# Optimization experiments

Measured on AMD Instinct MI355X. Metric: run time of the kernel, lower is better.

Reference implementation:

```python
import jax, jax.numpy as jnp
import numpy as np

N, E, IN, HID, H, OUT = 50000, 800000, 128, 64, 4, 128
NEG = 0.2   # LeakyReLU slope in GATv2
EPS = 1e-5  # BatchNorm eps


def _seg_softmax(a, seg, n):
    # numerically stable softmax over edges grouped by destination node
    amax = jax.lax.stop_gradient(jax.ops.segment_max(a, seg, num_segments=n))
    amax = jnp.where(jnp.isfinite(amax), amax, 0.0)
    ex = jnp.exp(a - amax[seg])
    den = jax.ops.segment_sum(ex, seg, num_segments=n)
    return ex / (den[seg] + 1e-16)


def _gatv2(x, src, dst, e_attr, Wl, bl, Wr, br, We, att, bias, heads, c, concat):
    n = x.shape[0]
    xl = (x @ Wl + bl).reshape(n, heads, c)   # source transform (x_j)
    xr = (x @ Wr + br).reshape(n, heads, c)   # target transform (x_i)
    ee = (e_attr @ We).reshape(-1, heads, c)  # edge feature transform
    m = xl[src] + xr[dst] + ee                # [E, H, C]
    m = jnp.where(m > 0, m, NEG * m)          # LeakyReLU
    alpha = _seg_softmax(jnp.einsum('ehc,hc->eh', m, att), dst, n)  # [E, H]
    out = jax.ops.segment_sum(alpha[:, :, None] * xl[src], dst, num_segments=n)
    out = out.reshape(n, heads * c) if concat else out.mean(axis=1)
    return out + bias


def _bn(h, g, b):  # BatchNorm1d, training-mode batch stats (biased var)
    mu = jnp.mean(h, axis=0)
    var = jnp.var(h, axis=0)
    return (h - mu) * jax.lax.rsqrt(var + EPS) * g + b


def _prelu(h, a):
    return jnp.where(h > 0, h, a * h)


def setup_inputs() -> dict:
    key = jax.random.key(0)
    ks = jax.random.split(key, 16)
    def nrm(k, shape, fan):
        return jax.random.normal(k, shape, jnp.float32) / np.float32(np.sqrt(fan))
    x = jax.random.normal(ks[0], (N, IN), jnp.float32)
    edge_index = jax.random.randint(ks[1], (2, E), 0, N, jnp.int32)
    edge_attr = jax.random.uniform(ks[2], (E, 1), dtype=jnp.float32)
    return {
        'x': x, 'edge_index': edge_index, 'edge_attr': edge_attr,
        # layer 1: heads=4, concat=True
        'Wl1': nrm(ks[3], (IN, H * HID), IN), 'bl1': jnp.zeros((H * HID,), jnp.float32),
        'Wr1': nrm(ks[4], (IN, H * HID), IN), 'br1': jnp.zeros((H * HID,), jnp.float32),
        'We1': nrm(ks[5], (1, H * HID), 1),
        'att1': nrm(ks[6], (H, HID), HID),
        'cb1': jnp.zeros((H * HID,), jnp.float32),
        'bng1': jnp.ones((H * HID,), jnp.float32), 'bnb1': jnp.zeros((H * HID,), jnp.float32),
        'pa': jnp.float32(0.25),  # PReLU single parameter (shared by both uses)
        # layer 2: heads=1, concat=False
        'Wl2': nrm(ks[7], (H * HID, OUT), H * HID), 'bl2': jnp.zeros((OUT,), jnp.float32),
        'Wr2': nrm(ks[8], (H * HID, OUT), H * HID), 'br2': jnp.zeros((OUT,), jnp.float32),
        'We2': nrm(ks[9], (1, OUT), 1),
        'att2': nrm(ks[10], (1, OUT), OUT),
        'cb2': jnp.zeros((OUT,), jnp.float32),
        'bng2': jnp.ones((OUT,), jnp.float32), 'bnb2': jnp.zeros((OUT,), jnp.float32),
        'skipW': nrm(ks[11], (IN, OUT), IN), 'skipb': jnp.zeros((OUT,), jnp.float32),
    }


def reference(x, edge_index, edge_attr, Wl1, bl1, Wr1, br1, We1, att1, cb1,
              bng1, bnb1, pa, Wl2, bl2, Wr2, br2, We2, att2, cb2, bng2, bnb2,
              skipW, skipb):
    src, dst = edge_index[0], edge_index[1]
    h = _gatv2(x, src, dst, edge_attr, Wl1, bl1, Wr1, br1, We1, att1, cb1, H, HID, True)
    h = _prelu(_bn(h, bng1, bnb1), pa)  # dropout = identity (eval)
    h = _gatv2(h, src, dst, edge_attr, Wl2, bl2, Wr2, br2, We2, att2, cb2, 1, OUT, False)
    h = _prelu(_bn(h, bng2, bnb2), pa)
    return h + (x @ skipW + skipb)
```

## Files before the change

kernel.cpp:

```cpp
#include <hip/hip_runtime.h>
#include <cstdint>
#include <cstddef>

#define NNODES 50000
#define NEDGES 800000
#define DH1    256
#define DOUT   128

typedef unsigned short u16;
typedef __bf16 bf16x8 __attribute__((ext_vector_type(8)));
typedef float  f32x4  __attribute__((ext_vector_type(4)));

__device__ __forceinline__ float bf2f(unsigned int u) {
  union { unsigned int i; float f; } x; x.i = u << 16; return x.f;
}
__device__ __forceinline__ u16 f2bf(float f) {
  union { float f; unsigned int i; } x; x.f = f;
  unsigned int r = x.i + 0x7fffu + ((x.i >> 16) & 1u);
  return (u16)(r >> 16);
}
__device__ __forceinline__ void dec8(uint4 r, float* o) {
  o[0] = bf2f(r.x & 0xffffu); o[1] = bf2f(r.x >> 16);
  o[2] = bf2f(r.y & 0xffffu); o[3] = bf2f(r.y >> 16);
  o[4] = bf2f(r.z & 0xffffu); o[5] = bf2f(r.z >> 16);
  o[6] = bf2f(r.w & 0xffffu); o[7] = bf2f(r.w >> 16);
}
__device__ __forceinline__ uint4 pack8(const float* v) {
  uint4 p;
  p.x = (unsigned)f2bf(v[0]) | ((unsigned)f2bf(v[1]) << 16);
  p.y = (unsigned)f2bf(v[2]) | ((unsigned)f2bf(v[3]) << 16);
  p.z = (unsigned)f2bf(v[4]) | ((unsigned)f2bf(v[5]) << 16);
  p.w = (unsigned)f2bf(v[6]) | ((unsigned)f2bf(v[7]) << 16);
  return p;
}


#define CNT_BLKS 3125
#define CVT_BLKS 6250
#define W1_BLKS  320
#define W2_BLKS  256

__global__ __launch_bounds__(256) void setup_k(
    const int* __restrict__ dst, int* __restrict__ cnt,
    const float* __restrict__ x, u16* __restrict__ xbf,
    const float* __restrict__ Wl1, const float* __restrict__ Wr1,
    const float* __restrict__ bl1, const float* __restrict__ br1,
    const float* __restrict__ Wl2, const float* __restrict__ Wr2,
    const float* __restrict__ bl2, const float* __restrict__ br2,
    const float* __restrict__ skW, const float* __restrict__ skb,
    const float* __restrict__ att1, const float* __restrict__ We1,
    const float* __restrict__ att2, const float* __restrict__ We2,
    u16* __restrict__ Wcat1, float* __restrict__ bias1,
    u16* __restrict__ Wt2, float* __restrict__ bias2,
    float* __restrict__ axw) {
  int b = blockIdx.x, t = threadIdx.x;
  if (b < CNT_BLKS) {
    int e = b * 256 + t;
    if (e < NEDGES) atomicAdd(&cnt[dst[e]], 1);
  } else if (b < CNT_BLKS + CVT_BLKS) {
    int i = ((b - CNT_BLKS) * 256 + t) * 4;
    float4 v = *reinterpret_cast<const float4*>(x + i);
    uint2 pk;
    pk.x = (unsigned)f2bf(v.x) | ((unsigned)f2bf(v.y) << 16);
    pk.y = (unsigned)f2bf(v.z) | ((unsigned)f2bf(v.w) << 16);
    *reinterpret_cast<uint2*>(xbf + i) = pk;
  } else if (b < CNT_BLKS + CVT_BLKS + W1_BLKS) {
    int idx = (b - CNT_BLKS - CVT_BLKS) * 256 + t;
    if (idx < 640) bias1[idx] = idx < 256 ? bl1[idx] : idx < 512 ? br1[idx - 256] : skb[idx - 512];
    int n = idx >> 7, k = idx & 127;
    float v = n < 256 ? Wl1[k * 256 + n] : n < 512 ? Wr1[k * 256 + (n - 256)] : skW[k * 128 + (n - 512)];
    Wcat1[idx] = f2bf(v);
  } else if (b < CNT_BLKS + CVT_BLKS + W1_BLKS + W2_BLKS) {
    int idx = (b - CNT_BLKS - CVT_BLKS - W1_BLKS) * 256 + t;
    if (idx < 256) bias2[idx] = idx < 128 ? bl2[idx] : br2[idx - 128];
    int n = idx >> 8, k = idx & 255;
    float v = n < 128 ? Wl2[k * 128 + n] : Wr2[k * 128 + (n - 128)];
    Wt2[idx] = f2bf(v);
  } else {
    if (t < 4) {
      float s = 0.f;
      for (int c = 0; c < 64; ++c) s += att1[t * 64 + c] * We1[t * 64 + c];
      axw[t] = s;
    } else if (t == 4) {
      float s = 0.f;
      for (int c = 0; c < 128; ++c) s += att2[c] * We2[c];
      axw[4] = s;
    }
  }
}


__global__ __launch_bounds__(256) void offsets_k(const int* __restrict__ cnt, int* __restrict__ offs,
                                                 int* __restrict__ cursor, int* __restrict__ total) {
  int i = blockIdx.x * 256 + threadIdx.x;
  int lane = threadIdx.x & 63;
  int c = (i < NNODES) ? cnt[i] : 0;
  int incl = c;
  #pragma unroll
  for (int d = 1; d < 64; d <<= 1) {
    int t = __shfl_up(incl, d, 64);
    if (lane >= d) incl += t;
  }
  int wtotal = __shfl(incl, 63, 64);
  int base = 0;
  if (lane == 63) base = atomicAdd(total, wtotal);
  base = __shfl(base, 63, 64);
  int off = base + incl - c;
  if (i < NNODES) { offs[i] = off; cursor[i] = off; }
}

__global__ __launch_bounds__(256) void scatter_k(const int* __restrict__ src, const int* __restrict__ dst,
                                                 const float* __restrict__ ea, int* __restrict__ cursor,
                                                 int2* __restrict__ epair) {
  int e = blockIdx.x * 256 + threadIdx.x;
  if (e >= NEDGES) return;
  int d = dst[e];
  int p = atomicAdd(&cursor[d], 1);
  int2 v; v.x = src[e]; v.y = __float_as_int(ea[e]);
  epair[p] = v;
}


template<int K, int B1, int B2, int LDC0, int LDC1, int LDC2, int SPAN, int ATTLEN, bool DO_ATT>
__global__ __launch_bounds__(512) void gemm_mfma(
    const u16* __restrict__ A, const u16* __restrict__ Wt, const float* __restrict__ bias,
    u16* __restrict__ C0, u16* __restrict__ C1, u16* __restrict__ C2,
    const float* __restrict__ att, float* __restrict__ axl, float* __restrict__ axr) {
  constexpr int LDA = K + 8;
  constexpr int CSTR = 136;
  constexpr size_t ABYTES = (size_t)64 * LDA * 2;
  constexpr size_t CBYTES = (size_t)64 * CSTR * 2;
  constexpr size_t SBYTES = ABYTES > CBYTES ? ABYTES : CBYTES;
  __shared__ __align__(16) char smem[SBYTES];
  __shared__ float attS[128];
  u16* As = (u16*)smem;
  const int row0 = blockIdx.x * 64;
  const int tid = threadIdx.x;
  #pragma unroll
  for (int it = 0; it < K / 32; ++it) {
    int chunk = it * 512 + tid;
    int row = (chunk * 4) / K;
    int col = (chunk * 4) % K;
    uint2 v; v.x = 0u; v.y = 0u;
    int gr = row0 + row;
    if (gr < NNODES) v = *reinterpret_cast<const uint2*>(A + (size_t)gr * K + col);
    *reinterpret_cast<uint2*>(&As[row * LDA + col]) = v;
  }
  __syncthreads();
  const int w = tid >> 6, lane = tid & 63, q = lane >> 4, l16 = lane & 15;
  const int tc = w * 16 + l16;
  const int cb = blockIdx.y * 128;
  const int ncol = cb + tc;
  f32x4 acc[4];
  #pragma unroll
  for (int rt = 0; rt < 4; ++rt) acc[rt] = (f32x4){0.f, 0.f, 0.f, 0.f};
  const u16* wp = Wt + (size_t)ncol * K + q * 8;
  #pragma unroll
  for (int ks = 0; ks < K / 32; ++ks) {
    bf16x8 b = *reinterpret_cast<const bf16x8*>(wp + ks * 32);
    #pragma unroll
    for (int rt = 0; rt < 4; ++rt) {
      bf16x8 a = *reinterpret_cast<const bf16x8*>(&As[(rt * 16 + l16) * LDA + ks * 32 + q * 8]);
      acc[rt] = __builtin_amdgcn_mfma_f32_16x16x32_bf16(a, b, acc[rt], 0, 0, 0);
    }
  }
  const float bval = bias[ncol];
  __syncthreads();
  u16* Cs = (u16*)smem;
  #pragma unroll
  for (int rt = 0; rt < 4; ++rt)
    #pragma unroll
    for (int r = 0; r < 4; ++r)
      Cs[(rt * 16 + q * 4 + r) * CSTR + tc] = f2bf(acc[rt][r] + bval);
  __syncthreads();
  {
    u16* Cg; int LD, cc;
    if (cb < B1)      { Cg = C0; LD = LDC0; cc = cb; }
    else if (cb < B2) { Cg = C1; LD = LDC1; cc = cb - B1; }
    else              { Cg = C2; LD = LDC2; cc = cb - B2; }
    #pragma unroll
    for (int it = 0; it < 2; ++it) {
      int ch = it * 512 + tid;
      int row = ch / 16, co = (ch % 16) * 8;
      int grow = row0 + row;
      if (grow < NNODES) {
        uint4 v = *reinterpret_cast<const uint4*>(&Cs[row * CSTR + co]);
        *reinterpret_cast<uint4*>(Cg + (size_t)grow * LD + cc + co) = v;
      }
    }
  }
  if constexpr (DO_ATT) {
    if (cb < B2) {
      if (tid < 128) attS[tid] = att[(cb + tid) % ATTLEN];
      __syncthreads();
      constexpr int TPR = 128 / SPAN;
      constexpr int HEADS = B1 / SPAN;
      if (tid < 64 * TPR) {
        int row = tid / TPR, hb = tid % TPR;
        const u16* cr = Cs + row * CSTR + hb * SPAN;
        float s = 0.f;
        for (int c = 0; c < SPAN; ++c) s += bf2f(cr[c]) * attS[hb * SPAN + c];
        int grow = row0 + row;
        if (grow < NNODES) {
          int cbl = cb < B1 ? cb : cb - B1;
          int lh = cbl / SPAN + hb;
          float* dstp = (cb < B1) ? axl : axr;
          dstp[grow * HEADS + lh] = s;
        }
      }
    }
  }
}


template<int HEADS, int CHAN, int EPW>
__global__ __launch_bounds__(256) void gat_edge(
    const int* __restrict__ offs, const int* __restrict__ cnt,
    const int2* __restrict__ epair,
    const u16* __restrict__ xl, const u16* __restrict__ xr,
    const float* __restrict__ att, const float* __restrict__ We,
    const float* __restrict__ cb,
    const float* __restrict__ axl, const float* __restrict__ axr,
    const float* __restrict__ aWep, u16* __restrict__ hout) {
  constexpr int HC  = HEADS * CHAN;
  constexpr int GSZ = 64 / EPW;
  constexpr int CPL = HC / GSZ;
  constexpr int LPH = CHAN / CPL;
  static_assert(CPL == 8, "layout");

  int node = __builtin_amdgcn_readfirstlane((int)(blockIdx.x * 4 + (threadIdx.x >> 6)));
  if (node >= NNODES) return;
  const int lane = threadIdx.x & 63;
  const int g    = lane / GSZ;
  const int lgs  = lane & (GSZ - 1);
  const int h    = lgs / LPH;
  const int cbase = lgs * CPL;

  float xrv[8], attv[8], wev[8];
  {
    uint4 xrr = *reinterpret_cast<const uint4*>(xr + (size_t)node * HC + cbase);
    dec8(xrr, xrv);
    float4 a0 = *reinterpret_cast<const float4*>(att + cbase);
    float4 a1 = *reinterpret_cast<const float4*>(att + cbase + 4);
    float4 w0 = *reinterpret_cast<const float4*>(We + cbase);
    float4 w1 = *reinterpret_cast<const float4*>(We + cbase + 4);
    attv[0]=a0.x; attv[1]=a0.y; attv[2]=a0.z; attv[3]=a0.w;
    attv[4]=a1.x; attv[5]=a1.y; attv[6]=a1.z; attv[7]=a1.w;
    wev[0]=w0.x; wev[1]=w0.y; wev[2]=w0.z; wev[3]=w0.w;
    wev[4]=w1.x; wev[5]=w1.y; wev[6]=w1.z; wev[7]=w1.w;
  }
  const float aWe = aWep[h];
  const float axr_n = axr[node * HEADS + h];
  const int off = __builtin_amdgcn_readfirstlane(offs[node]);
  const int deg = __builtin_amdgcn_readfirstlane(cnt[node]);

  float den = 0.f;
  float accv[8];
  #pragma unroll
  for (int c = 0; c < 8; ++c) accv[c] = 0.f;

  if (deg > 0) {
    const int last = deg - 1;
    auto midx = [&](int i) { int j = i * EPW + g; return off + (j < last ? j : last); };
    int2 p_cur = epair[midx(0)];
    int2 p_nxt = epair[midx(1)];
    uint4 r_cur; float ax_cur;
    { int s = p_cur.x;
      r_cur = *reinterpret_cast<const uint4*>(xl + (size_t)s * HC + cbase);
      ax_cur = axl[s * HEADS + h]; }
    const int niter = (deg + EPW - 1) / EPW;
    for (int i = 0; i < niter; ++i) {
      int2 p_n2 = epair[midx(i + 2)];
      uint4 r_n; float ax_n;
      { int s = p_nxt.x;
        r_n = *reinterpret_cast<const uint4*>(xl + (size_t)s * HC + cbase);
        ax_n = axl[s * HEADS + h]; }
      float ea = __int_as_float(p_cur.y);
      float xlv[8];
      dec8(r_cur, xlv);
      float part2 = 0.f;
      #pragma unroll
      for (int c = 0; c < 8; ++c) {
        float m = xlv[c] + fmaf(ea, wev[c], xrv[c]);
        part2 = fmaf(fabsf(m), attv[c], part2);
      }
      #pragma unroll
      for (int d = 1; d < LPH; d <<= 1) part2 += __shfl_xor(part2, d, 64);
      float ssum = ax_cur + fmaf(ea, aWe, axr_n);
      float sc = fmaf(0.4f, part2, 0.6f * ssum);
      float e = __expf(sc);
      e = (i * EPW + g <= last) ? e : 0.f;
      den += e;
      #pragma unroll
      for (int c = 0; c < 8; ++c) accv[c] = fmaf(e, xlv[c], accv[c]);
      p_cur = p_nxt; p_nxt = p_n2; r_cur = r_n; ax_cur = ax_n;
    }
  }
  #pragma unroll
  for (int d = GSZ; d < 64; d <<= 1) {
    den += __shfl_xor(den, d, 64);
    #pragma unroll
    for (int c = 0; c < 8; ++c) accv[c] += __shfl_xor(accv[c], d, 64);
  }
  if (g == 0) {
    float inv = 1.0f / (den + 1e-16f);
    float4 c0 = *reinterpret_cast<const float4*>(cb + cbase);
    float4 c1 = *reinterpret_cast<const float4*>(cb + cbase + 4);
    float ov[8];
    ov[0] = accv[0] * inv + c0.x; ov[1] = accv[1] * inv + c0.y;
    ov[2] = accv[2] * inv + c0.z; ov[3] = accv[3] * inv + c0.w;
    ov[4] = accv[4] * inv + c1.x; ov[5] = accv[5] * inv + c1.y;
    ov[6] = accv[6] * inv + c1.z; ov[7] = accv[7] * inv + c1.w;
    *reinterpret_cast<uint4*>(hout + (size_t)node * HC + cbase) = pack8(ov);
  }
}


template<int NC>
__global__ void bn_stats_bf(const u16* __restrict__ h, float* __restrict__ sum, float* __restrict__ sq) {
  int c = threadIdx.x;
  float s = 0.f, q = 0.f;
  for (int r = blockIdx.x; r < NNODES; r += gridDim.x) {
    float v = bf2f(h[(size_t)r * NC + c]);
    s += v; q += v * v;
  }
  atomicAdd(&sum[c], s);
  atomicAdd(&sq[c], q);
}

template<int NC>
__global__ __launch_bounds__(256) void bn_prelu_apply(
    const u16* __restrict__ h, const float* __restrict__ sum, const float* __restrict__ sq,
    const float* __restrict__ g, const float* __restrict__ bb_,
    const float* __restrict__ pap, u16* __restrict__ outp, int total) {
  int i = (blockIdx.x * 256 + threadIdx.x) * 4;
  if (i >= total) return;
  const float invN = 1.0f / (float)NNODES;
  float pa = pap[0];
  int c = i & (NC - 1);
  float4 sm = *reinterpret_cast<const float4*>(sum + c);
  float4 qq = *reinterpret_cast<const float4*>(sq + c);
  float4 gg = *reinterpret_cast<const float4*>(g + c);
  float4 bb = *reinterpret_cast<const float4*>(bb_ + c);
  float mu, var, sc[4], sh[4];
  mu = sm.x * invN; var = qq.x * invN - mu * mu; sc[0] = gg.x * rsqrtf(var + 1e-5f); sh[0] = bb.x - mu * sc[0];
  mu = sm.y * invN; var = qq.y * invN - mu * mu; sc[1] = gg.y * rsqrtf(var + 1e-5f); sh[1] = bb.y - mu * sc[1];
  mu = sm.z * invN; var = qq.z * invN - mu * mu; sc[2] = gg.z * rsqrtf(var + 1e-5f); sh[2] = bb.z - mu * sc[2];
  mu = sm.w * invN; var = qq.w * invN - mu * mu; sc[3] = gg.w * rsqrtf(var + 1e-5f); sh[3] = bb.w - mu * sc[3];
  uint2 raw = *reinterpret_cast<const uint2*>(h + i);
  float v0 = bf2f(raw.x & 0xffffu), v1 = bf2f(raw.x >> 16);
  float v2 = bf2f(raw.y & 0xffffu), v3 = bf2f(raw.y >> 16);
  float o0 = v0 * sc[0] + sh[0]; o0 = o0 > 0.f ? o0 : pa * o0;
  float o1 = v1 * sc[1] + sh[1]; o1 = o1 > 0.f ? o1 : pa * o1;
  float o2 = v2 * sc[2] + sh[2]; o2 = o2 > 0.f ? o2 : pa * o2;
  float o3 = v3 * sc[3] + sh[3]; o3 = o3 > 0.f ? o3 : pa * o3;
  uint2 pk;
  pk.x = (unsigned)f2bf(o0) | ((unsigned)f2bf(o1) << 16);
  pk.y = (unsigned)f2bf(o2) | ((unsigned)f2bf(o3) << 16);
  *reinterpret_cast<uint2*>(outp + i) = pk;
}

__global__ __launch_bounds__(256) void final_out_k(
    const u16* __restrict__ h2, const u16* __restrict__ skip,
    const float* __restrict__ sum, const float* __restrict__ sq,
    const float* __restrict__ g, const float* __restrict__ bb_,
    const float* __restrict__ pap, float* __restrict__ outp, int total) {
  int i = (blockIdx.x * 256 + threadIdx.x) * 4;
  if (i >= total) return;
  const float invN = 1.0f / (float)NNODES;
  float pa = pap[0];
  int c = i & 127;
  float4 sm = *reinterpret_cast<const float4*>(sum + c);
  float4 qq = *reinterpret_cast<const float4*>(sq + c);
  float4 gg = *reinterpret_cast<const float4*>(g + c);
  float4 bb = *reinterpret_cast<const float4*>(bb_ + c);
  float mu, var, sc[4], sh[4];
  mu = sm.x * invN; var = qq.x * invN - mu * mu; sc[0] = gg.x * rsqrtf(var + 1e-5f); sh[0] = bb.x - mu * sc[0];
  mu = sm.y * invN; var = qq.y * invN - mu * mu; sc[1] = gg.y * rsqrtf(var + 1e-5f); sh[1] = bb.y - mu * sc[1];
  mu = sm.z * invN; var = qq.z * invN - mu * mu; sc[2] = gg.z * rsqrtf(var + 1e-5f); sh[2] = bb.z - mu * sc[2];
  mu = sm.w * invN; var = qq.w * invN - mu * mu; sc[3] = gg.w * rsqrtf(var + 1e-5f); sh[3] = bb.w - mu * sc[3];
  uint2 raw = *reinterpret_cast<const uint2*>(h2 + i);
  float v0 = bf2f(raw.x & 0xffffu), v1 = bf2f(raw.x >> 16);
  float v2 = bf2f(raw.y & 0xffffu), v3 = bf2f(raw.y >> 16);
  uint2 skr = *reinterpret_cast<const uint2*>(skip + i);
  float s0 = bf2f(skr.x & 0xffffu), s1 = bf2f(skr.x >> 16);
  float s2 = bf2f(skr.y & 0xffffu), s3 = bf2f(skr.y >> 16);
  float4 o;
  o.x = v0 * sc[0] + sh[0]; o.x = (o.x > 0.f ? o.x : pa * o.x) + s0;
  o.y = v1 * sc[1] + sh[1]; o.y = (o.y > 0.f ? o.y : pa * o.y) + s1;
  o.z = v2 * sc[2] + sh[2]; o.z = (o.z > 0.f ? o.z : pa * o.z) + s2;
  o.w = v3 * sc[3] + sh[3]; o.w = (o.w > 0.f ? o.w : pa * o.w) + s3;
  *reinterpret_cast<float4*>(outp + i) = o;
}


extern "C" void kernel_launch(void* const* d_in, const int* in_sizes, int n_in,
                              void* d_out, int out_size, void* d_ws, size_t ws_size,
                              hipStream_t stream) {
  (void)in_sizes; (void)n_in; (void)out_size; (void)ws_size;
  const float* x    = (const float*)d_in[0];
  const int*   ei   = (const int*)d_in[1];
  const float* ea   = (const float*)d_in[2];
  const float* Wl1  = (const float*)d_in[3];
  const float* bl1  = (const float*)d_in[4];
  const float* Wr1  = (const float*)d_in[5];
  const float* br1  = (const float*)d_in[6];
  const float* We1  = (const float*)d_in[7];
  const float* att1 = (const float*)d_in[8];
  const float* cb1  = (const float*)d_in[9];
  const float* bng1 = (const float*)d_in[10];
  const float* bnb1 = (const float*)d_in[11];
  const float* pa   = (const float*)d_in[12];
  const float* Wl2  = (const float*)d_in[13];
  const float* bl2  = (const float*)d_in[14];
  const float* Wr2  = (const float*)d_in[15];
  const float* br2  = (const float*)d_in[16];
  const float* We2  = (const float*)d_in[17];
  const float* att2 = (const float*)d_in[18];
  const float* cb2  = (const float*)d_in[19];
  const float* bng2 = (const float*)d_in[20];
  const float* bnb2 = (const float*)d_in[21];
  const float* skW  = (const float*)d_in[22];
  const float* skb  = (const float*)d_in[23];
  const int* srcp = ei;
  const int* dstp = ei + NEDGES;

  char* base = (char*)d_ws;
  size_t off = 0;
  auto alloc = [&](size_t bytes) -> char* {
    char* p = base + off;
    off = (off + bytes + 255) & ~(size_t)255;
    return p;
  };
  size_t zero_ints = 1 + NNODES + 256 + 256 + 128 + 128;
  char* zbase = alloc(zero_ints * 4);
  int*   totalp = (int*)zbase;
  int*   cnt    = totalp + 1;
  float* bnsum1 = (float*)(cnt + NNODES);
  float* bnsq1  = bnsum1 + 256;
  float* bnsum2 = bnsq1 + 256;
  float* bnsq2  = bnsum2 + 128;

  int*   offs    = (int*)alloc((size_t)NNODES * 4);
  int*   cursor  = (int*)alloc((size_t)NNODES * 4);
  int2*  epair   = (int2*)alloc((size_t)NEDGES * 8);
  const size_t RBYTES = (size_t)NNODES * DH1 * 2;
  char* regionA = alloc(RBYTES);
  char* regionB = alloc(RBYTES);
  char* regionC = alloc(RBYTES);
  u16*   xbf    = (u16*)alloc((size_t)NNODES * 128 * 2);
  u16*   skipbf = (u16*)alloc((size_t)NNODES * 128 * 2);
  u16*   Wcat1  = (u16*)alloc(640 * 128 * 2);
  u16*   Wt2    = (u16*)alloc(256 * 256 * 2);
  float* bias1  = (float*)alloc(640 * 4);
  float* bias2  = (float*)alloc(256 * 4);
  float* axw    = (float*)alloc(8 * 4);
  float* axl1   = (float*)alloc((size_t)NNODES * 4 * 4);
  float* axr1   = (float*)alloc((size_t)NNODES * 4 * 4);
  float* axl2   = (float*)alloc((size_t)NNODES * 4);
  float* axr2   = (float*)alloc((size_t)NNODES * 4);

  u16*   xl1     = (u16*)regionA;
  u16*   xr1     = (u16*)regionB;
  u16*   h1      = (u16*)regionC;
  u16*   h1p     = (u16*)regionA;
  u16*   xl2     = (u16*)regionC;
  u16*   xr2     = (u16*)(regionC + (size_t)NNODES * DOUT * 2);
  u16*   h2      = (u16*)regionA;

  hipMemsetAsync(zbase, 0, zero_ints * 4, stream);

  const int EB = (NEDGES + 255) / 256;
  const int NB = (NNODES + 255) / 256;
  setup_k<<<CNT_BLKS + CVT_BLKS + W1_BLKS + W2_BLKS + 1, 256, 0, stream>>>(
      dstp, cnt, x, xbf, Wl1, Wr1, bl1, br1, Wl2, Wr2, bl2, br2, skW, skb,
      att1, We1, att2, We2, Wcat1, bias1, Wt2, bias2, axw);
  offsets_k<<<NB, 256, 0, stream>>>(cnt, offs, cursor, totalp);
  scatter_k<<<EB, 256, 0, stream>>>(srcp, dstp, ea, cursor, epair);

  const int MB64 = (NNODES + 63) / 64;
  gemm_mfma<128, 256, 512, 256, 256, 128, 64, 256, true><<<dim3(MB64, 5), 512, 0, stream>>>(
      xbf, Wcat1, bias1, xl1, xr1, skipbf, att1, axl1, axr1);
  gat_edge<4, 64, 2><<<(NNODES + 3) / 4, 256, 0, stream>>>(
      offs, cnt, epair, xl1, xr1, att1, We1, cb1, axl1, axr1, axw, h1);
  bn_stats_bf<256><<<800, 256, 0, stream>>>(h1, bnsum1, bnsq1);
  bn_prelu_apply<256><<<(NNODES * DH1 / 4 + 255) / 256, 256, 0, stream>>>(
      h1, bnsum1, bnsq1, bng1, bnb1, pa, h1p, NNODES * DH1);

  gemm_mfma<256, 128, 256, 128, 128, 1, 128, 128, true><<<dim3(MB64, 2), 512, 0, stream>>>(
      h1p, Wt2, bias2, xl2, xr2, (u16*)0, att2, axl2, axr2);
  gat_edge<1, 128, 4><<<(NNODES + 3) / 4, 256, 0, stream>>>(
      offs, cnt, epair, xl2, xr2, att2, We2, cb2, axl2, axr2, axw + 4, h2);
  bn_stats_bf<128><<<800, 128, 0, stream>>>(h2, bnsum2, bnsq2);
  final_out_k<<<(NNODES * DOUT / 4 + 255) / 256, 256, 0, stream>>>(
      h2, skipbf, bnsum2, bnsq2, bng2, bnb2, pa, (float*)d_out, NNODES * DOUT);
}
```

Before: 491.9 us.

## Reuse count-atomic ranks for CSR scatter and pack edge math into v_pk_fma

```diff
diff --git a/kernel.cpp b/kernel.cpp
--- a/kernel.cpp
+++ b/kernel.cpp
@@ -18,12 +18,6 @@
   union { float f; unsigned int i; } x; x.f = f;
   unsigned int r = x.i + 0x7fffu + ((x.i >> 16) & 1u);
   return (u16)(r >> 16);
-}
-__device__ __forceinline__ void dec8(uint4 r, float* o) {
-  o[0] = bf2f(r.x & 0xffffu); o[1] = bf2f(r.x >> 16);
-  o[2] = bf2f(r.y & 0xffffu); o[3] = bf2f(r.y >> 16);
-  o[4] = bf2f(r.z & 0xffffu); o[5] = bf2f(r.z >> 16);
-  o[6] = bf2f(r.w & 0xffffu); o[7] = bf2f(r.w >> 16);
 }
 __device__ __forceinline__ uint4 pack8(const float* v) {
   uint4 p;
@@ -34,6 +28,27 @@
   return p;
 }
 
+__device__ __forceinline__ float2 pkfma(float2 a, float2 b, float2 c) {
+  float2 d;
+  asm("v_pk_fma_f32 %0, %1, %2, %3" : "=v"(d) : "v"(a), "v"(b), "v"(c));
+  return d;
+}
+__device__ __forceinline__ float2 pkadd(float2 a, float2 b) {
+  float2 d;
+  asm("v_pk_add_f32 %0, %1, %2" : "=v"(d) : "v"(a), "v"(b));
+  return d;
+}
+__device__ __forceinline__ float2 abs2(float2 a) {
+  union { float2 f; uint2 u; } x; x.f = a;
+  x.u.x &= 0x7fffffffu; x.u.y &= 0x7fffffffu;
+  return x.f;
+}
+__device__ __forceinline__ float2 dec2(unsigned u) {
+  union { unsigned i; float f; } lo, hi;
+  lo.i = u << 16; hi.i = u & 0xffff0000u;
+  float2 d; d.x = lo.f; d.y = hi.f; return d;
+}
+
 
 #define CNT_BLKS 3125
 #define CVT_BLKS 6250
@@ -41,7 +56,7 @@
 #define W2_BLKS  256
 
 __global__ __launch_bounds__(256) void setup_k(
-    const int* __restrict__ dst, int* __restrict__ cnt,
+    const int* __restrict__ dst, int* __restrict__ cnt, int* __restrict__ rank,
     const float* __restrict__ x, u16* __restrict__ xbf,
     const float* __restrict__ Wl1, const float* __restrict__ Wr1,
     const float* __restrict__ bl1, const float* __restrict__ br1,
@@ -56,7 +71,7 @@
   int b = blockIdx.x, t = threadIdx.x;
   if (b < CNT_BLKS) {
     int e = b * 256 + t;
-    if (e < NEDGES) atomicAdd(&cnt[dst[e]], 1);
+    if (e < NEDGES) rank[e] = atomicAdd(&cnt[dst[e]], 1);
   } else if (b < CNT_BLKS + CVT_BLKS) {
     int i = ((b - CNT_BLKS) * 256 + t) * 4;
     float4 v = *reinterpret_cast<const float4*>(x + i);
@@ -91,7 +106,7 @@
 
 
 __global__ __launch_bounds__(256) void offsets_k(const int* __restrict__ cnt, int* __restrict__ offs,
-                                                 int* __restrict__ cursor, int* __restrict__ total) {
+                                                 int* __restrict__ total) {
   int i = blockIdx.x * 256 + threadIdx.x;
   int lane = threadIdx.x & 63;
   int c = (i < NNODES) ? cnt[i] : 0;
@@ -106,16 +121,15 @@
   if (lane == 63) base = atomicAdd(total, wtotal);
   base = __shfl(base, 63, 64);
   int off = base + incl - c;
-  if (i < NNODES) { offs[i] = off; cursor[i] = off; }
+  if (i < NNODES) offs[i] = off;
 }
 
 __global__ __launch_bounds__(256) void scatter_k(const int* __restrict__ src, const int* __restrict__ dst,
-                                                 const float* __restrict__ ea, int* __restrict__ cursor,
-                                                 int2* __restrict__ epair) {
+                                                 const float* __restrict__ ea, const int* __restrict__ offs,
+                                                 const int* __restrict__ rank, int2* __restrict__ epair) {
   int e = blockIdx.x * 256 + threadIdx.x;
   if (e >= NEDGES) return;
-  int d = dst[e];
-  int p = atomicAdd(&cursor[d], 1);
+  int p = offs[dst[e]] + rank[e];
   int2 v; v.x = src[e]; v.y = __float_as_int(ea[e]);
   epair[p] = v;
 }
@@ -236,18 +250,19 @@
   const int h    = lgs / LPH;
   const int cbase = lgs * CPL;
 
-  float xrv[8], attv[8], wev[8];
+  float2 xrv2[4], attv2[4], wev2[4];
   {
     uint4 xrr = *reinterpret_cast<const uint4*>(xr + (size_t)node * HC + cbase);
-    dec8(xrr, xrv);
+    xrv2[0] = dec2(xrr.x); xrv2[1] = dec2(xrr.y);
+    xrv2[2] = dec2(xrr.z); xrv2[3] = dec2(xrr.w);
     float4 a0 = *reinterpret_cast<const float4*>(att + cbase);
     float4 a1 = *reinterpret_cast<const float4*>(att + cbase + 4);
     float4 w0 = *reinterpret_cast<const float4*>(We + cbase);
     float4 w1 = *reinterpret_cast<const float4*>(We + cbase + 4);
-    attv[0]=a0.x; attv[1]=a0.y; attv[2]=a0.z; attv[3]=a0.w;
-    attv[4]=a1.x; attv[5]=a1.y; attv[6]=a1.z; attv[7]=a1.w;
-    wev[0]=w0.x; wev[1]=w0.y; wev[2]=w0.z; wev[3]=w0.w;
-    wev[4]=w1.x; wev[5]=w1.y; wev[6]=w1.z; wev[7]=w1.w;
+    attv2[0].x=a0.x; attv2[0].y=a0.y; attv2[1].x=a0.z; attv2[1].y=a0.w;
+    attv2[2].x=a1.x; attv2[2].y=a1.y; attv2[3].x=a1.z; attv2[3].y=a1.w;
+    wev2[0].x=w0.x; wev2[0].y=w0.y; wev2[1].x=w0.z; wev2[1].y=w0.w;
+    wev2[2].x=w1.x; wev2[2].y=w1.y; wev2[3].x=w1.z; wev2[3].y=w1.w;
   }
   const float aWe = aWep[h];
   const float axr_n = axr[node * HEADS + h];
@@ -255,9 +270,9 @@
   const int deg = __builtin_amdgcn_readfirstlane(cnt[node]);
 
   float den = 0.f;
-  float accv[8];
-  #pragma unroll
-  for (int c = 0; c < 8; ++c) accv[c] = 0.f;
+  float2 acc2[4];
+  #pragma unroll
+  for (int c = 0; c < 4; ++c) { acc2[c].x = 0.f; acc2[c].y = 0.f; }
 
   if (deg > 0) {
     const int last = deg - 1;
@@ -276,14 +291,17 @@
         r_n = *reinterpret_cast<const uint4*>(xl + (size_t)s * HC + cbase);
         ax_n = axl[s * HEADS + h]; }
       float ea = __int_as_float(p_cur.y);
-      float xlv[8];
-      dec8(r_cur, xlv);
-      float part2 = 0.f;
+      float2 xl2[4];
+      xl2[0] = dec2(r_cur.x); xl2[1] = dec2(r_cur.y);
+      xl2[2] = dec2(r_cur.z); xl2[3] = dec2(r_cur.w);
+      float2 ea2; ea2.x = ea; ea2.y = ea;
+      float2 dot2; dot2.x = 0.f; dot2.y = 0.f;
       #pragma unroll
-      for (int c = 0; c < 8; ++c) {
-        float m = xlv[c] + fmaf(ea, wev[c], xrv[c]);
-        part2 = fmaf(fabsf(m), attv[c], part2);
+      for (int c = 0; c < 4; ++c) {
+        float2 m = pkadd(xl2[c], pkfma(ea2, wev2[c], xrv2[c]));
+        dot2 = pkfma(abs2(m), attv2[c], dot2);
       }
+      float part2 = dot2.x + dot2.y;
       #pragma unroll
       for (int d = 1; d < LPH; d <<= 1) part2 += __shfl_xor(part2, d, 64);
       float ssum = ax_cur + fmaf(ea, aWe, axr_n);
@@ -291,8 +309,9 @@
       float e = __expf(sc);
       e = (i * EPW + g <= last) ? e : 0.f;
       den += e;
+      float2 e2; e2.x = e; e2.y = e;
       #pragma unroll
-      for (int c = 0; c < 8; ++c) accv[c] = fmaf(e, xlv[c], accv[c]);
+      for (int c = 0; c < 4; ++c) acc2[c] = pkfma(e2, xl2[c], acc2[c]);
       p_cur = p_nxt; p_nxt = p_n2; r_cur = r_n; ax_cur = ax_n;
     }
   }
@@ -300,17 +319,20 @@
   for (int d = GSZ; d < 64; d <<= 1) {
     den += __shfl_xor(den, d, 64);
     #pragma unroll
-    for (int c = 0; c < 8; ++c) accv[c] += __shfl_xor(accv[c], d, 64);
+    for (int c = 0; c < 4; ++c) {
+      acc2[c].x += __shfl_xor(acc2[c].x, d, 64);
+      acc2[c].y += __shfl_xor(acc2[c].y, d, 64);
+    }
   }
   if (g == 0) {
     float inv = 1.0f / (den + 1e-16f);
     float4 c0 = *reinterpret_cast<const float4*>(cb + cbase);
     float4 c1 = *reinterpret_cast<const float4*>(cb + cbase + 4);
     float ov[8];
-    ov[0] = accv[0] * inv + c0.x; ov[1] = accv[1] * inv + c0.y;
-    ov[2] = accv[2] * inv + c0.z; ov[3] = accv[3] * inv + c0.w;
-    ov[4] = accv[4] * inv + c1.x; ov[5] = accv[5] * inv + c1.y;
-    ov[6] = accv[6] * inv + c1.z; ov[7] = accv[7] * inv + c1.w;
+    ov[0] = acc2[0].x * inv + c0.x; ov[1] = acc2[0].y * inv + c0.y;
+    ov[2] = acc2[1].x * inv + c0.z; ov[3] = acc2[1].y * inv + c0.w;
+    ov[4] = acc2[2].x * inv + c1.x; ov[5] = acc2[2].y * inv + c1.y;
+    ov[6] = acc2[3].x * inv + c1.z; ov[7] = acc2[3].y * inv + c1.w;
     *reinterpret_cast<uint4*>(hout + (size_t)node * HC + cbase) = pack8(ov);
   }
 }
@@ -442,7 +464,7 @@
   float* bnsq2  = bnsum2 + 128;
 
   int*   offs    = (int*)alloc((size_t)NNODES * 4);
-  int*   cursor  = (int*)alloc((size_t)NNODES * 4);
+  int*   rank    = (int*)alloc((size_t)NEDGES * 4);
   int2*  epair   = (int2*)alloc((size_t)NEDGES * 8);
   const size_t RBYTES = (size_t)NNODES * DH1 * 2;
   char* regionA = alloc(RBYTES);
@@ -473,10 +495,10 @@
   const int EB = (NEDGES + 255) / 256;
   const int NB = (NNODES + 255) / 256;
   setup_k<<<CNT_BLKS + CVT_BLKS + W1_BLKS + W2_BLKS + 1, 256, 0, stream>>>(
-      dstp, cnt, x, xbf, Wl1, Wr1, bl1, br1, Wl2, Wr2, bl2, br2, skW, skb,
+      dstp, cnt, rank, x, xbf, Wl1, Wr1, bl1, br1, Wl2, Wr2, bl2, br2, skW, skb,
       att1, We1, att2, We2, Wcat1, bias1, Wt2, bias2, axw);
-  offsets_k<<<NB, 256, 0, stream>>>(cnt, offs, cursor, totalp);
-  scatter_k<<<EB, 256, 0, stream>>>(srcp, dstp, ea, cursor, epair);
+  offsets_k<<<NB, 256, 0, stream>>>(cnt, offs, totalp);
+  scatter_k<<<EB, 256, 0, stream>>>(srcp, dstp, ea, offs, rank, epair);
 
   const int MB64 = (NNODES + 63) / 64;
   gemm_mfma<128, 256, 512, 256, 256, 128, 64, 256, true><<<dim3(MB64, 5), 512, 0, stream>>>(
```

New measurement: 471.8 us. 1.04x faster.

## Fuse BN+PReLU into layer-2 GEMM prologue and replace scatter atomics with ranks

Applied to the files above, without the earlier changes.

```diff
diff --git a/kernel.cpp b/kernel.cpp
--- a/kernel.cpp
+++ b/kernel.cpp
@@ -41,7 +41,7 @@
 #define W2_BLKS  256
 
 __global__ __launch_bounds__(256) void setup_k(
-    const int* __restrict__ dst, int* __restrict__ cnt,
+    const int* __restrict__ dst, int* __restrict__ cnt, int* __restrict__ rank,
     const float* __restrict__ x, u16* __restrict__ xbf,
     const float* __restrict__ Wl1, const float* __restrict__ Wr1,
     const float* __restrict__ bl1, const float* __restrict__ br1,
@@ -56,7 +56,7 @@
   int b = blockIdx.x, t = threadIdx.x;
   if (b < CNT_BLKS) {
     int e = b * 256 + t;
-    if (e < NEDGES) atomicAdd(&cnt[dst[e]], 1);
+    if (e < NEDGES) rank[e] = atomicAdd(&cnt[dst[e]], 1);
   } else if (b < CNT_BLKS + CVT_BLKS) {
     int i = ((b - CNT_BLKS) * 256 + t) * 4;
     float4 v = *reinterpret_cast<const float4*>(x + i);
@@ -91,7 +91,7 @@
 
 
 __global__ __launch_bounds__(256) void offsets_k(const int* __restrict__ cnt, int* __restrict__ offs,
-                                                 int* __restrict__ cursor, int* __restrict__ total) {
+                                                 int* __restrict__ total) {
   int i = blockIdx.x * 256 + threadIdx.x;
   int lane = threadIdx.x & 63;
   int c = (i < NNODES) ? cnt[i] : 0;
@@ -106,16 +106,15 @@
   if (lane == 63) base = atomicAdd(total, wtotal);
   base = __shfl(base, 63, 64);
   int off = base + incl - c;
-  if (i < NNODES) { offs[i] = off; cursor[i] = off; }
+  if (i < NNODES) offs[i] = off;
 }
 
 __global__ __launch_bounds__(256) void scatter_k(const int* __restrict__ src, const int* __restrict__ dst,
-                                                 const float* __restrict__ ea, int* __restrict__ cursor,
-                                                 int2* __restrict__ epair) {
+                                                 const float* __restrict__ ea, const int* __restrict__ offs,
+                                                 const int* __restrict__ rank, int2* __restrict__ epair) {
   int e = blockIdx.x * 256 + threadIdx.x;
   if (e >= NEDGES) return;
-  int d = dst[e];
-  int p = atomicAdd(&cursor[d], 1);
+  int p = offs[dst[e]] + rank[e];
   int2 v; v.x = src[e]; v.y = __float_as_int(ea[e]);
   epair[p] = v;
 }
@@ -207,6 +206,112 @@
           float* dstp = (cb < B1) ? axl : axr;
           dstp[grow * HEADS + lh] = s;
         }
+      }
+    }
+  }
+}
+
+
+__global__ __launch_bounds__(512) void gemm2_bn(
+    const u16* __restrict__ A, const u16* __restrict__ Wt, const float* __restrict__ bias,
+    u16* __restrict__ C0, u16* __restrict__ C1,
+    const float* __restrict__ att, float* __restrict__ axl, float* __restrict__ axr,
+    const float* __restrict__ bnsum, const float* __restrict__ bnsq,
+    const float* __restrict__ bng, const float* __restrict__ bnb,
+    const float* __restrict__ pap) {
+  constexpr int K = 256, B1 = 128;
+  constexpr int LDA = K + 8;
+  constexpr int CSTR = 136;
+  __shared__ __align__(16) char smem[(size_t)64 * LDA * 2];
+  __shared__ float attS[128];
+  __shared__ float scS[256], shS[256];
+  u16* As = (u16*)smem;
+  const int tid = threadIdx.x;
+  const int row0 = blockIdx.x * 64;
+  const float pa = pap[0];
+  if (tid < 256) {
+    const float invN = 1.0f / (float)NNODES;
+    float mu = bnsum[tid] * invN;
+    float var = bnsq[tid] * invN - mu * mu;
+    float s = bng[tid] * rsqrtf(var + 1e-5f);
+    scS[tid] = s;
+    shS[tid] = bnb[tid] - mu * s;
+  }
+  __syncthreads();
+  #pragma unroll
+  for (int it = 0; it < K / 32; ++it) {
+    int chunk = it * 512 + tid;
+    int row = chunk / 64;
+    int col = (chunk % 64) * 4;
+    uint2 v; v.x = 0u; v.y = 0u;
+    int gr = row0 + row;
+    if (gr < NNODES) v = *reinterpret_cast<const uint2*>(A + (size_t)gr * K + col);
+    float o0 = bf2f(v.x & 0xffffu) * scS[col]     + shS[col];
+    float o1 = bf2f(v.x >> 16)     * scS[col + 1] + shS[col + 1];
+    float o2 = bf2f(v.y & 0xffffu) * scS[col + 2] + shS[col + 2];
+    float o3 = bf2f(v.y >> 16)     * scS[col + 3] + shS[col + 3];
+    o0 = o0 > 0.f ? o0 : pa * o0;
+    o1 = o1 > 0.f ? o1 : pa * o1;
+    o2 = o2 > 0.f ? o2 : pa * o2;
+    o3 = o3 > 0.f ? o3 : pa * o3;
+    uint2 pk;
+    pk.x = (unsigned)f2bf(o0) | ((unsigned)f2bf(o1) << 16);
+    pk.y = (unsigned)f2bf(o2) | ((unsigned)f2bf(o3) << 16);
+    *reinterpret_cast<uint2*>(&As[row * LDA + col]) = pk;
+  }
+  __syncthreads();
+  const int w = tid >> 6, lane = tid & 63, q = lane >> 4, l16 = lane & 15;
+  const int tc = w * 16 + l16;
+  const int cb = blockIdx.y * 128;
+  const int ncol = cb + tc;
+  f32x4 acc[4];
+  #pragma unroll
+  for (int rt = 0; rt < 4; ++rt) acc[rt] = (f32x4){0.f, 0.f, 0.f, 0.f};
+  const u16* wp = Wt + (size_t)ncol * K + q * 8;
+  #pragma unroll
+  for (int ks = 0; ks < K / 32; ++ks) {
+    bf16x8 b = *reinterpret_cast<const bf16x8*>(wp + ks * 32);
+    #pragma unroll
+    for (int rt = 0; rt < 4; ++rt) {
+      bf16x8 a = *reinterpret_cast<const bf16x8*>(&As[(rt * 16 + l16) * LDA + ks * 32 + q * 8]);
+      acc[rt] = __builtin_amdgcn_mfma_f32_16x16x32_bf16(a, b, acc[rt], 0, 0, 0);
+    }
+  }
+  const float bval = bias[ncol];
+  __syncthreads();
+  u16* Cs = (u16*)smem;
+  #pragma unroll
+  for (int rt = 0; rt < 4; ++rt)
+    #pragma unroll
+    for (int r = 0; r < 4; ++r)
+      Cs[(rt * 16 + q * 4 + r) * CSTR + tc] = f2bf(acc[rt][r] + bval);
+  __syncthreads();
+  {
+    u16* Cg = (cb < B1) ? C0 : C1;
+    int cc = (cb < B1) ? cb : cb - B1;
+    #pragma unroll
+    for (int it = 0; it < 2; ++it) {
+      int ch = it * 512 + tid;
+      int row = ch / 16, co = (ch % 16) * 8;
+      int grow = row0 + row;
+      if (grow < NNODES) {
+        uint4 v = *reinterpret_cast<const uint4*>(&Cs[row * CSTR + co]);
+        *reinterpret_cast<uint4*>(Cg + (size_t)grow * 128 + cc + co) = v;
+      }
+    }
+  }
+  {
+    if (tid < 128) attS[tid] = att[(cb + tid) % 128];
+    __syncthreads();
+    if (tid < 64) {
+      int row = tid;
+      const u16* cr = Cs + row * CSTR;
+      float s = 0.f;
+      for (int c = 0; c < 128; ++c) s += bf2f(cr[c]) * attS[c];
+      int grow = row0 + row;
+      if (grow < NNODES) {
+        float* dstp = (cb < B1) ? axl : axr;
+        dstp[grow] = s;
       }
     }
   }
@@ -328,38 +433,6 @@
   atomicAdd(&sq[c], q);
 }
 
-template<int NC>
-__global__ __launch_bounds__(256) void bn_prelu_apply(
-    const u16* __restrict__ h, const float* __restrict__ sum, const float* __restrict__ sq,
-    const float* __restrict__ g, const float* __restrict__ bb_,
-    const float* __restrict__ pap, u16* __restrict__ outp, int total) {
-  int i = (blockIdx.x * 256 + threadIdx.x) * 4;
-  if (i >= total) return;
-  const float invN = 1.0f / (float)NNODES;
-  float pa = pap[0];
-  int c = i & (NC - 1);
-  float4 sm = *reinterpret_cast<const float4*>(sum + c);
-  float4 qq = *reinterpret_cast<const float4*>(sq + c);
-  float4 gg = *reinterpret_cast<const float4*>(g + c);
-  float4 bb = *reinterpret_cast<const float4*>(bb_ + c);
-  float mu, var, sc[4], sh[4];
-  mu = sm.x * invN; var = qq.x * invN - mu * mu; sc[0] = gg.x * rsqrtf(var + 1e-5f); sh[0] = bb.x - mu * sc[0];
-  mu = sm.y * invN; var = qq.y * invN - mu * mu; sc[1] = gg.y * rsqrtf(var + 1e-5f); sh[1] = bb.y - mu * sc[1];
-  mu = sm.z * invN; var = qq.z * invN - mu * mu; sc[2] = gg.z * rsqrtf(var + 1e-5f); sh[2] = bb.z - mu * sc[2];
-  mu = sm.w * invN; var = qq.w * invN - mu * mu; sc[3] = gg.w * rsqrtf(var + 1e-5f); sh[3] = bb.w - mu * sc[3];
-  uint2 raw = *reinterpret_cast<const uint2*>(h + i);
-  float v0 = bf2f(raw.x & 0xffffu), v1 = bf2f(raw.x >> 16);
-  float v2 = bf2f(raw.y & 0xffffu), v3 = bf2f(raw.y >> 16);
-  float o0 = v0 * sc[0] + sh[0]; o0 = o0 > 0.f ? o0 : pa * o0;
-  float o1 = v1 * sc[1] + sh[1]; o1 = o1 > 0.f ? o1 : pa * o1;
-  float o2 = v2 * sc[2] + sh[2]; o2 = o2 > 0.f ? o2 : pa * o2;
-  float o3 = v3 * sc[3] + sh[3]; o3 = o3 > 0.f ? o3 : pa * o3;
-  uint2 pk;
-  pk.x = (unsigned)f2bf(o0) | ((unsigned)f2bf(o1) << 16);
-  pk.y = (unsigned)f2bf(o2) | ((unsigned)f2bf(o3) << 16);
-  *reinterpret_cast<uint2*>(outp + i) = pk;
-}
-
 __global__ __launch_bounds__(256) void final_out_k(
     const u16* __restrict__ h2, const u16* __restrict__ skip,
     const float* __restrict__ sum, const float* __restrict__ sq,
@@ -442,7 +515,7 @@
   float* bnsq2  = bnsum2 + 128;
 
   int*   offs    = (int*)alloc((size_t)NNODES * 4);
-  int*   cursor  = (int*)alloc((size_t)NNODES * 4);
+  int*   rank    = (int*)alloc((size_t)NEDGES * 4);
   int2*  epair   = (int2*)alloc((size_t)NEDGES * 8);
   const size_t RBYTES = (size_t)NNODES * DH1 * 2;
   char* regionA = alloc(RBYTES);
@@ -463,9 +536,8 @@
   u16*   xl1     = (u16*)regionA;
   u16*   xr1     = (u16*)regionB;
   u16*   h1      = (u16*)regionC;
-  u16*   h1p     = (u16*)regionA;
-  u16*   xl2     = (u16*)regionC;
-  u16*   xr2     = (u16*)(regionC + (size_t)NNODES * DOUT * 2);
+  u16*   xl2     = (u16*)regionB;
+  u16*   xr2     = (u16*)(regionB + (size_t)NNODES * DOUT * 2);
   u16*   h2      = (u16*)regionA;
 
   hipMemsetAsync(zbase, 0, zero_ints * 4, stream);
@@ -473,10 +545,10 @@
   const int EB = (NEDGES + 255) / 256;
   const int NB = (NNODES + 255) / 256;
   setup_k<<<CNT_BLKS + CVT_BLKS + W1_BLKS + W2_BLKS + 1, 256, 0, stream>>>(
-      dstp, cnt, x, xbf, Wl1, Wr1, bl1, br1, Wl2, Wr2, bl2, br2, skW, skb,
+      dstp, cnt, rank, x, xbf, Wl1, Wr1, bl1, br1, Wl2, Wr2, bl2, br2, skW, skb,
       att1, We1, att2, We2, Wcat1, bias1, Wt2, bias2, axw);
-  offsets_k<<<NB, 256, 0, stream>>>(cnt, offs, cursor, totalp);
-  scatter_k<<<EB, 256, 0, stream>>>(srcp, dstp, ea, cursor, epair);
+  offsets_k<<<NB, 256, 0, stream>>>(cnt, offs, totalp);
+  scatter_k<<<EB, 256, 0, stream>>>(srcp, dstp, ea, offs, rank, epair);
 
   const int MB64 = (NNODES + 63) / 64;
   gemm_mfma<128, 256, 512, 256, 256, 128, 64, 256, true><<<dim3(MB64, 5), 512, 0, stream>>>(
@@ -484,11 +556,9 @@
   gat_edge<4, 64, 2><<<(NNODES + 3) / 4, 256, 0, stream>>>(
       offs, cnt, epair, xl1, xr1, att1, We1, cb1, axl1, axr1, axw, h1);
   bn_stats_bf<256><<<800, 256, 0, stream>>>(h1, bnsum1, bnsq1);
-  bn_prelu_apply<256><<<(NNODES * DH1 / 4 + 255) / 256, 256, 0, stream>>>(
-      h1, bnsum1, bnsq1, bng1, bnb1, pa, h1p, NNODES * DH1);
-
-  gemm_mfma<256, 128, 256, 128, 128, 1, 128, 128, true><<<dim3(MB64, 2), 512, 0, stream>>>(
-      h1p, Wt2, bias2, xl2, xr2, (u16*)0, att2, axl2, axr2);
+
+  gemm2_bn<<<dim3(MB64, 2), 512, 0, stream>>>(
+      h1, Wt2, bias2, xl2, xr2, att2, axl2, axr2, bnsum1, bnsq1, bng1, bnb1, pa);
   gat_edge<1, 128, 4><<<(NNODES + 3) / 4, 256, 0, stream>>>(
       offs, cnt, epair, xl2, xr2, att2, We2, cb2, axl2, axr2, axw + 4, h2);
   bn_stats_bf<128><<<800, 128, 0, stream>>>(h2, bnsum2, bnsq2);
```

After: 448.2 us. 8.9% less time.
